# Kernel optimization log

Measured on AMD Instinct MI355X. Metric: run time of the kernel, lower is better.

The kernel has to match this reference:

```python
import jax, jax.numpy as jnp
import numpy as np
from jax import lax

B, E, D, N, R, K = 4, 768, 1536, 16, 48, 4
H, W = 16, 16
L = H * W
NDIR = 4


def _perms():
    idx = np.arange(L)
    idx_v = np.arange(L).reshape(H, W).T.reshape(-1)  # column-major (vertical) scan order
    perms = [idx, idx[::-1].copy(), idx_v, idx_v[::-1].copy()]
    invs = [np.argsort(p) for p in perms]
    return [jnp.asarray(p) for p in perms], [jnp.asarray(p) for p in invs]

PERMS, INVS = _perms()


def setup_inputs() -> dict:
    key = jax.random.key(0)
    ks = jax.random.split(key, 10)
    hidden_states = jax.random.normal(ks[0], (B, L, E), jnp.float32)
    in_proj_w = jax.random.normal(ks[1], (2 * D, E), jnp.float32) * 0.02
    out_proj_w = jax.random.normal(ks[2], (E, D), jnp.float32) * 0.02
    conv_w = jax.random.normal(ks[3], (NDIR, D, K), jnp.float32) * 0.1
    conv_b = jax.random.normal(ks[4], (NDIR, D), jnp.float32) * 0.1
    xproj_w = jax.random.normal(ks[5], (NDIR, R + 2 * N, D), jnp.float32) * 0.02
    dt_init_std = R ** -0.5
    dtproj_w = jax.random.uniform(ks[6], (NDIR, D, R), jnp.float32, -dt_init_std, dt_init_std)
    dt = jnp.exp(jax.random.uniform(ks[7], (NDIR, D), jnp.float32)
                 * (np.log(0.1) - np.log(0.001)) + np.log(0.001))
    dt = jnp.clip(dt, 1e-4, None)
    dtproj_b = dt + jnp.log(-jnp.expm1(-dt))  # inverse-softplus init as in the module
    A_log = jnp.broadcast_to(
        jnp.log(jnp.arange(1, N + 1, dtype=jnp.float32))[None, None, :], (NDIR, D, N)).copy()
    D_param = jnp.ones((NDIR, D), jnp.float32)
    return dict(hidden_states=hidden_states, in_proj_w=in_proj_w, out_proj_w=out_proj_w,
                conv_w=conv_w, conv_b=conv_b, xproj_w=xproj_w, dtproj_w=dtproj_w,
                dtproj_b=dtproj_b, A_log=A_log, D_param=D_param)


def _mamba_dir(xz, cw, cb, xw, dtw, dtb, a_log, dpar):
    # xz: (B, 2D, L) in this direction's scan order
    x, z = xz[:, :D], xz[:, D:]
    # causal depthwise conv1d + SiLU (mamba_inner_fn conv path)
    x = lax.conv_general_dilated(x, cw[:, None, :], (1,), [(K - 1, 0)],
                                 feature_group_count=D,
                                 dimension_numbers=('NCH', 'OIH', 'NCH'))
    x = jax.nn.silu(x + cb[None, :, None])
    # x_proj -> dt, B, C
    x_dbl = jnp.einsum('bdl,kd->bkl', x, xw)
    dt, Bm, Cm = x_dbl[:, :R], x_dbl[:, R:R + N], x_dbl[:, R + N:]
    delta = jax.nn.softplus(jnp.einsum('brl,dr->bdl', dt, dtw) + dtb[None, :, None])
    A = -jnp.exp(a_log)                                  # (D, N)
    dA = jnp.exp(jnp.einsum('bdl,dn->lbdn', delta, A))   # (L, B, D, N)
    dBu = jnp.einsum('bdl,bnl,bdl->lbdn', delta, Bm, x)  # delta * B * u

    def step(h, inp):
        da, dbu = inp
        h = da * h + dbu
        return h, h

    h0 = jnp.zeros((x.shape[0], D, N), x.dtype)
    _, hs = lax.scan(step, h0, (dA, dBu))                # (L, B, D, N)
    y = jnp.einsum('lbdn,bnl->bdl', hs, Cm) + dpar[None, :, None] * x
    return y * jax.nn.silu(z)                            # gate, (B, D, L)


def reference(hidden_states, in_proj_w, out_proj_w, conv_w, conv_b,
              xproj_w, dtproj_w, dtproj_b, A_log, D_param):
    xz = jnp.einsum('ble,fe->bfl', hidden_states, in_proj_w)  # (B, 2D, L)
    out = jnp.zeros((hidden_states.shape[0], D, L), hidden_states.dtype)
    for i in range(NDIR):  # fixed small set of structurally distinct scan directions
        xz_i = xz[:, :, PERMS[i]]
        y = _mamba_dir(xz_i, conv_w[i], conv_b[i], xproj_w[i], dtproj_w[i],
                       dtproj_b[i], A_log[i], D_param[i])
        out = out + y[:, :, INVS[i]]  # multi_reverse then sum-fusion
    return jnp.einsum('bdl,ed->ble', out, out_proj_w)
```

## Files before the change

### kernel.cpp

```cpp
#include <hip/hip_runtime.h>
#include <hip/hip_bf16.h>

#define BI   4
#define LI   256
#define EI   768
#define DI   1536
#define NI   16
#define RI   48
#define KI   4
#define NDIRS 4
#define F2D  3072
#define MROWS 1024
#define LOG2E 1.4426950408889634f

typedef float    floatx2 __attribute__((ext_vector_type(2)));
typedef float    floatx4 __attribute__((ext_vector_type(4)));
typedef _Float16 halfx2  __attribute__((ext_vector_type(2)));
typedef _Float16 halfx4  __attribute__((ext_vector_type(4)));
typedef _Float16 halfx8  __attribute__((ext_vector_type(8)));

typedef __attribute__((address_space(3))) unsigned lds_u32;
typedef __attribute__((address_space(1))) const unsigned glb_u32;

__device__ __forceinline__ void load16(const _Float16* g, _Float16* l) {
    __builtin_amdgcn_global_load_lds((glb_u32*)g, (lds_u32*)l, 16, 0, 0);
}

__device__ __forceinline__ int perm_idx(int dir, int j) {
    switch (dir) {
        case 0:  return j;
        case 1:  return 255 - j;
        case 2:  return ((j & 15) << 4) | (j >> 4);
        default: return 255 - (((j & 15) << 4) | (j >> 4));
    }
}

template<int CTRL>
__device__ __forceinline__ float dpp_add(float p) {
    int t = __builtin_amdgcn_update_dpp(0, __builtin_bit_cast(int, p),
                                        CTRL, 0xf, 0xf, true);
    return p + __builtin_bit_cast(float, t);
}
__device__ __forceinline__ float grp8_sum(float p) {
    p = dpp_add<0xB1>(p);
    p = dpp_add<0x4E>(p);
    p = dpp_add<0x141>(p);
    return p;
}

template<int BM, int BN, int WGN, int FM, int FN>
__device__ __forceinline__ void gemm_core(const _Float16* __restrict__ Ah,
                                          const _Float16* __restrict__ Al, int lda,
                                          const _Float16* __restrict__ Bh,
                                          const _Float16* __restrict__ Bl, int ldb,
                                          int nChunks, _Float16* smem,
                                          floatx4 (&acc)[FM][FN]) {
    const int tid = threadIdx.x, lane = tid & 63, wave = tid >> 6;
    const int wave_m = wave / WGN, wave_n = wave % WGN;
    _Float16* sAh = smem;
    _Float16* sAl = smem + BM * 32;
    _Float16* sBh = smem + BM * 64;
    _Float16* sBl = smem + BM * 64 + BN * 32;
    const int rr = lane & 15, koff = (lane >> 4) * 8;
    const int arow = wave_m * FM * 16, brow = wave_n * FN * 16;

    for (int c = 0; c < nChunks; ++c) {
        for (int idx = tid; idx < BM * 4; idx += 256) {
            int r = idx >> 2, s = (idx & 3) * 8;
            load16(Ah + (size_t)r * lda + c * 32 + s, sAh + idx * 8);
            load16(Al + (size_t)r * lda + c * 32 + s, sAl + idx * 8);
        }
        for (int idx = tid; idx < BN * 4; idx += 256) {
            int r = idx >> 2, s = (idx & 3) * 8;
            load16(Bh + (size_t)r * ldb + c * 32 + s, sBh + idx * 8);
            load16(Bl + (size_t)r * ldb + c * 32 + s, sBl + idx * 8);
        }
        asm volatile("s_waitcnt vmcnt(0)" ::: "memory");
        __syncthreads();

        halfx8 ahf[FM], alf[FM], bhf[FN], blf[FN];
        #pragma unroll
        for (int i = 0; i < FM; ++i) {
            ahf[i] = *(const halfx8*)(sAh + (arow + i * 16 + rr) * 32 + koff);
            alf[i] = *(const halfx8*)(sAl + (arow + i * 16 + rr) * 32 + koff);
        }
        #pragma unroll
        for (int j = 0; j < FN; ++j) {
            bhf[j] = *(const halfx8*)(sBh + (brow + j * 16 + rr) * 32 + koff);
            blf[j] = *(const halfx8*)(sBl + (brow + j * 16 + rr) * 32 + koff);
        }
        #pragma unroll
        for (int i = 0; i < FM; ++i)
            #pragma unroll
            for (int j = 0; j < FN; ++j) {
                acc[i][j] = __builtin_amdgcn_mfma_f32_16x16x32_f16(ahf[i], bhf[j], acc[i][j], 0, 0, 0);
                acc[i][j] = __builtin_amdgcn_mfma_f32_16x16x32_f16(ahf[i], blf[j], acc[i][j], 0, 0, 0);
                acc[i][j] = __builtin_amdgcn_mfma_f32_16x16x32_f16(alf[i], bhf[j], acc[i][j], 0, 0, 0);
            }
        __syncthreads();
    }
}

__global__ __launch_bounds__(256) void k_splitall(
        const float* __restrict__ hs,  const float* __restrict__ wip,
        const float* __restrict__ wop, const float* __restrict__ xw,
        const float* __restrict__ dtw,
        _Float16* __restrict__ hsh,  _Float16* __restrict__ hsl,
        _Float16* __restrict__ wiph, _Float16* __restrict__ wipl,
        _Float16* __restrict__ woph, _Float16* __restrict__ wopl,
        _Float16* __restrict__ xwh,  _Float16* __restrict__ xwl,
        _Float16* __restrict__ dtwh, _Float16* __restrict__ dtwl) {
    int i4 = (blockIdx.x * 256 + threadIdx.x) * 4;
    floatx4 v;
    _Float16 *dh, *dl; int off;
    if (i4 < 786432)        { off = i4;           v = *(const floatx4*)(hs + off);  dh = hsh;  dl = hsl;  }
    else if (i4 < 3145728)  { off = i4 - 786432;  v = *(const floatx4*)(wip + off); dh = wiph; dl = wipl; }
    else if (i4 < 4325376)  { off = i4 - 3145728; v = *(const floatx4*)(wop + off); dh = woph; dl = wopl; }
    else if (i4 < 4816896)  { off = i4 - 4325376; v = *(const floatx4*)(xw + off);  dh = xwh;  dl = xwl;  }
    else {
        int t0 = i4 - 4816896;
        int col = t0 & 63, dr = t0 >> 6;
        floatx4 z = {0.f, 0.f, 0.f, 0.f};
        v = (col < 48) ? *(const floatx4*)(dtw + (size_t)dr * 48 + col) : z;
        dh = dtwh; dl = dtwl; off = t0;
    }
    halfx4 hh, hl;
    #pragma unroll
    for (int e = 0; e < 4; ++e) {
        _Float16 h = (_Float16)v[e];
        hh[e] = h; hl[e] = (_Float16)(v[e] - (float)h);
    }
    *(halfx4*)(dh + off) = hh;
    *(halfx4*)(dl + off) = hl;
}

__global__ __launch_bounds__(256) void k_inproj_t(const _Float16* __restrict__ Ah,
                                                  const _Float16* __restrict__ Al,
                                                  const _Float16* __restrict__ Bh,
                                                  const _Float16* __restrict__ Bl,
                                                  float* __restrict__ C) {
    __shared__ _Float16 smem[128 * 64 + 128 * 64];
    int row0 = blockIdx.x * 128, col0 = blockIdx.y * 128, k0 = blockIdx.z * 384;
    float* Cp = C + (size_t)blockIdx.z * MROWS * F2D;
    floatx4 acc[4][4] = {};
    gemm_core<128, 128, 2, 4, 4>(Ah + (size_t)row0 * EI + k0, Al + (size_t)row0 * EI + k0, EI,
                                 Bh + (size_t)col0 * EI + k0, Bl + (size_t)col0 * EI + k0, EI,
                                 12, smem, acc);
    int lane = threadIdx.x & 63, wave = threadIdx.x >> 6;
    int cc = lane & 15, q = lane >> 4;
    int rbase = row0 + (wave >> 1) * 64, cbase = col0 + (wave & 1) * 64;
    #pragma unroll
    for (int i = 0; i < 4; ++i)
        #pragma unroll
        for (int j = 0; j < 4; ++j)
            #pragma unroll
            for (int r = 0; r < 4; ++r)
                Cp[(size_t)(rbase + i * 16 + q * 4 + r) * F2D + cbase + j * 16 + cc] = acc[i][j][r];
}

__global__ __launch_bounds__(256) void k_outproj_t(const _Float16* __restrict__ Ah,
                                                   const _Float16* __restrict__ Al,
                                                   const _Float16* __restrict__ Bh,
                                                   const _Float16* __restrict__ Bl,
                                                   float* __restrict__ C) {
    __shared__ _Float16 smem[192 * 64];
    int row0 = blockIdx.x * 64, col0 = blockIdx.y * 128, k0 = blockIdx.z * 384;
    float* Cp = C + (size_t)blockIdx.z * MROWS * EI;
    floatx4 acc[2][4] = {};
    gemm_core<64, 128, 2, 2, 4>(Ah + (size_t)row0 * DI + k0, Al + (size_t)row0 * DI + k0, DI,
                                Bh + (size_t)col0 * DI + k0, Bl + (size_t)col0 * DI + k0, DI,
                                12, smem, acc);
    int lane = threadIdx.x & 63, wave = threadIdx.x >> 6;
    int cc = lane & 15, q = lane >> 4;
    int rbase = row0 + (wave >> 1) * 32, cbase = col0 + (wave & 1) * 64;
    #pragma unroll
    for (int i = 0; i < 2; ++i)
        #pragma unroll
        for (int j = 0; j < 4; ++j)
            #pragma unroll
            for (int r = 0; r < 4; ++r)
                Cp[(size_t)(rbase + i * 16 + q * 4 + r) * EI + cbase + j * 16 + cc] = acc[i][j][r];
}

__global__ __launch_bounds__(256) void k_osum(const float* __restrict__ oacc,
                                              float* __restrict__ out) {
    int i4 = (blockIdx.x * 256 + threadIdx.x) * 4;
    const size_t S = (size_t)MROWS * EI;
    floatx4 s = *(const floatx4*)(oacc + i4) + *(const floatx4*)(oacc + S + i4) +
                *(const floatx4*)(oacc + 2 * S + i4) + *(const floatx4*)(oacc + 3 * S + i4);
    *(floatx4*)(out + i4) = s;
}

__global__ __launch_bounds__(256) void k_xdbl_t(const _Float16* __restrict__ xh,
                                                const _Float16* __restrict__ xl,
                                                const _Float16* __restrict__ xwh,
                                                const _Float16* __restrict__ xwl,
                                                float* __restrict__ C) {
    __shared__ _Float16 smem[208 * 64];
    int row0 = blockIdx.x * 128, dir = blockIdx.y, k0 = blockIdx.z * 192;
    float* Cp = C + (size_t)blockIdx.z * NDIRS * MROWS * 80;
    floatx4 acc[2][5] = {};
    const size_t abase = ((size_t)dir * MROWS + row0) * DI + k0;
    const size_t bbase = (size_t)dir * 80 * DI + k0;
    gemm_core<128, 80, 1, 2, 5>(xh + abase, xl + abase, DI,
                                xwh + bbase, xwl + bbase, DI, 6, smem, acc);
    int lane = threadIdx.x & 63, wave = threadIdx.x >> 6;
    int cc = lane & 15, q = lane >> 4;
    int rbase = row0 + wave * 32;
    #pragma unroll
    for (int i = 0; i < 2; ++i)
        #pragma unroll
        for (int j = 0; j < 5; ++j)
            #pragma unroll
            for (int r = 0; r < 4; ++r)
                Cp[((size_t)dir * MROWS + rbase + i * 16 + q * 4 + r) * 80 + j * 16 + cc] = acc[i][j][r];
}

__global__ __launch_bounds__(256) void k_xsplit(const float* __restrict__ acc,
                                                _Float16* __restrict__ dtqh,
                                                _Float16* __restrict__ dtql,
                                                float* __restrict__ BCm) {
    const size_t PS = (size_t)NDIRS * MROWS * 80;
    int idx = blockIdx.x * 256 + threadIdx.x;
    int dir = idx / (MROWS * 96);
    int rem = idx - dir * MROWS * 96;
    int row = rem / 96, col = rem - row * 96;
    size_t rbase = (size_t)dir * MROWS + row;
    auto sum8 = [&](int c) {
        size_t o = rbase * 80 + c;
        float s = 0.f;
        #pragma unroll
        for (int kp = 0; kp < 8; ++kp) s += acc[kp * PS + o];
        return s;
    };
    if (col < 64) {
        float v = (col < 48) ? sum8(col) : 0.f;
        _Float16 h = (_Float16)v;
        dtqh[rbase * 64 + col] = h;
        dtql[rbase * 64 + col] = (_Float16)(v - (float)h);
    } else if (col < 80) {
        int n = col - 64;
        BCm[rbase * 32 + n * 2] = sum8(48 + n);
    } else {
        int n = col - 80;
        BCm[rbase * 32 + n * 2 + 1] = sum8(64 + n);
    }
}

__global__ __launch_bounds__(256) void k_delta_t(const _Float16* __restrict__ dtqh,
                                                 const _Float16* __restrict__ dtql,
                                                 const _Float16* __restrict__ dtwh,
                                                 const _Float16* __restrict__ dtwl,
                                                 const float* __restrict__ dtb,
                                                 float* __restrict__ delta) {
    __shared__ _Float16 smem[192 * 64];
    int row0 = blockIdx.x * 64, col0 = blockIdx.y * 128, dir = blockIdx.z;
    floatx4 acc[2][4] = {};
    const size_t abase = ((size_t)dir * MROWS + row0) * 64;
    const size_t bbase = ((size_t)dir * DI + col0) * 64;
    gemm_core<64, 128, 2, 2, 4>(dtqh + abase, dtql + abase, 64,
                                dtwh + bbase, dtwl + bbase, 64, 2, smem, acc);
    int lane = threadIdx.x & 63, wave = threadIdx.x >> 6;
    int cc = lane & 15, q = lane >> 4;
    int rbase = row0 + (wave >> 1) * 32, cbase = col0 + (wave & 1) * 64;
    #pragma unroll
    for (int i = 0; i < 2; ++i)
        #pragma unroll
        for (int j = 0; j < 4; ++j) {
            int col = cbase + j * 16 + cc;
            float bias = dtb[(size_t)dir * DI + col];
            #pragma unroll
            for (int r = 0; r < 4; ++r) {
                float v = acc[i][j][r] + bias;
                float sp = (v > 20.f) ? v : log1pf(__expf(v));
                delta[((size_t)dir * MROWS + rbase + i * 16 + q * 4 + r) * DI + col] = sp;
            }
        }
}

__global__ __launch_bounds__(256) void k_conv(const float* __restrict__ xz,
                                              const float* __restrict__ cw,
                                              const float* __restrict__ cb,
                                              _Float16* __restrict__ xh,
                                              _Float16* __restrict__ xl) {
    const size_t S = (size_t)MROWS * F2D;
    int dir = blockIdx.z, b = blockIdx.y;
    int lchunk = blockIdx.x / 6, dsub = blockIdx.x % 6;
    int d = dsub * 256 + threadIdx.x;
    int base = lchunk * 16;

    const float* w = cw + ((size_t)dir * DI + d) * KI;
    float w0 = w[0], w1 = w[1], w2 = w[2], w3 = w[3];
    float bias = cb[(size_t)dir * DI + d];

    auto ld = [&](int m) -> float {
        if (m < 0) return 0.f;
        int src = perm_idx(dir, m);
        size_t o = ((size_t)b * 256 + src) * F2D + d;
        return xz[o] + xz[S + o];
    };
    float xm3 = ld(base - 3), xm2 = ld(base - 2), xm1 = ld(base - 1);

    #pragma unroll
    for (int j = 0; j < 16; ++j) {
        float cur = ld(base + j);
        float s = bias + w0 * xm3 + w1 * xm2 + w2 * xm1 + w3 * cur;
        xm3 = xm2; xm2 = xm1; xm1 = cur;
        float x = s / (1.f + __expf(-s));
        _Float16 h = (_Float16)x;
        size_t o = ((size_t)dir * MROWS + b * 256 + base + j) * DI + d;
        xh[o] = h;
        xl[o] = (_Float16)(x - (float)h);
    }
}

__global__ __launch_bounds__(256) void k_scan(const float* __restrict__ delta,
                                              const _Float16* __restrict__ xhg,
                                              const _Float16* __restrict__ xlg,
                                              const float* __restrict__ BCm,
                                              const float* __restrict__ A_log,
                                              const float* __restrict__ Dp,
                                              float* __restrict__ ydir) {
    const int dchunk = blockIdx.x, b = blockIdx.y, dir = blockIdx.z;
    const int tid = threadIdx.x;
    const int dslot = tid >> 3;
    const int np = tid & 7;
    const int d0 = dchunk * 32, d = d0 + dslot;

    __shared__ float sdx[2][32][64];
    __shared__ float sbc[2][32][32];
    __shared__ float sY[32][32];

    const float Av0 = -__expf(A_log[((size_t)dir * DI + d) * NI + 2 * np]) * LOG2E;
    const float Av1 = -__expf(A_log[((size_t)dir * DI + d) * NI + 2 * np + 1]) * LOG2E;
    const float Dpar = Dp[(size_t)dir * DI + d];
    float h0 = 0.f, h1 = 0.f;

    const size_t dirrow = (size_t)dir * MROWS;
    const int srow = tid >> 3, sc4 = (tid & 7) * 4;

    floatx4 rdel, rbc;
    halfx4 rxh, rxl;
    auto load_chunk = [&](int j0) {
        int row = b * 256 + j0 + srow;
        size_t o = (dirrow + row) * DI + d0 + sc4;
        rdel = *(const floatx4*)(delta + o);
        rxh  = *(const halfx4*)(xhg + o);
        rxl  = *(const halfx4*)(xlg + o);
        rbc  = *(const floatx4*)(BCm + (dirrow + row) * 32 + sc4);
    };

    load_chunk(0);

    for (int c = 0; c < 8; ++c) {
        const int buf = c & 1;
        #pragma unroll
        for (int e = 0; e < 4; ++e) {
            sdx[buf][srow][(sc4 + e) * 2]     = rdel[e];
            sdx[buf][srow][(sc4 + e) * 2 + 1] = (float)rxh[e] + (float)rxl[e];
        }
        *(floatx4*)&sbc[buf][srow][sc4] = rbc;
        __syncthreads();
        if (c < 7) load_chunk((c + 1) * 32);

        #pragma unroll
        for (int jj = 0; jj < 32; ++jj) {
            floatx2 dx = *(const floatx2*)&sdx[buf][jj][dslot * 2];
            floatx4 bc = *(const floatx4*)&sbc[buf][jj][np * 4];
            float dv = dx[0], xv = dx[1];
            float a0 = __builtin_amdgcn_exp2f(dv * Av0);
            float a1 = __builtin_amdgcn_exp2f(dv * Av1);
            float du = dv * xv;
            h0 = fmaf(a0, h0, du * bc[0]);
            h1 = fmaf(a1, h1, du * bc[2]);
            float p = fmaf(h1, bc[3], h0 * bc[1]);
            p = grp8_sum(p);
            if (np == 0) sY[jj][dslot] = fmaf(Dpar, xv, p);
        }
        __syncthreads();

        {
            int lout = perm_idx(dir, c * 32 + srow);
            floatx4 o = *(const floatx4*)&sY[srow][sc4];
            *(floatx4*)&ydir[(dirrow + (size_t)b * 256 + lout) * DI + d0 + sc4] = o;
        }
    }
}

__global__ __launch_bounds__(256) void k_sum(const float* __restrict__ ydir,
                                             const float* __restrict__ xz,
                                             _Float16* __restrict__ yh,
                                             _Float16* __restrict__ yl) {
    int i4 = (blockIdx.x * 256 + threadIdx.x) * 4;
    const size_t S = (size_t)MROWS * DI;
    const size_t SZ = (size_t)MROWS * F2D;
    int row = i4 / DI, dcol = i4 - row * DI;
    size_t zo = (size_t)row * F2D + DI + dcol;
    floatx4 zv = *(const floatx4*)(xz + zo) + *(const floatx4*)(xz + SZ + zo);
    floatx4 s = *(const floatx4*)(ydir + i4) + *(const floatx4*)(ydir + S + i4) +
                *(const floatx4*)(ydir + 2 * S + i4) + *(const floatx4*)(ydir + 3 * S + i4);
    halfx4 hh, hl;
    #pragma unroll
    for (int e = 0; e < 4; ++e) {
        float g = zv[e] / (1.f + __expf(-zv[e]));
        float v = s[e] * g;
        _Float16 h = (_Float16)v;
        hh[e] = h; hl[e] = (_Float16)(v - (float)h);
    }
    *(halfx4*)(yh + i4) = hh;
    *(halfx4*)(yl + i4) = hl;
}

extern "C" void kernel_launch(void* const* d_in, const int* in_sizes, int n_in,
                              void* d_out, int out_size, void* d_ws, size_t ws_size,
                              hipStream_t stream) {
    const float* hs   = (const float*)d_in[0];
    const float* wip  = (const float*)d_in[1];
    const float* wop  = (const float*)d_in[2];
    const float* cw   = (const float*)d_in[3];
    const float* cb   = (const float*)d_in[4];
    const float* xw   = (const float*)d_in[5];
    const float* dtw  = (const float*)d_in[6];
    const float* dtb  = (const float*)d_in[7];
    const float* alog = (const float*)d_in[8];
    const float* dpar = (const float*)d_in[9];
    float* out = (float*)d_out;

    char* p = (char*)d_ws;
    auto alloc_f32 = [&](size_t n) { float* r = (float*)p; p += n * 4; return r; };
    auto alloc_f16 = [&](size_t n) { _Float16* r = (_Float16*)p; p += n * 2; return r; };

    _Float16* hsh  = alloc_f16(786432);
    _Float16* hsl  = alloc_f16(786432);
    _Float16* wiph = alloc_f16(2359296);
    _Float16* wipl = alloc_f16(2359296);
    _Float16* woph = alloc_f16(1179648);
    _Float16* wopl = alloc_f16(1179648);
    _Float16* xwh  = alloc_f16(491520);
    _Float16* xwl  = alloc_f16(491520);
    _Float16* dtwh = alloc_f16((size_t)NDIRS * DI * 64);
    _Float16* dtwl = alloc_f16((size_t)NDIRS * DI * 64);
    float*    xz   = alloc_f32((size_t)2 * MROWS * F2D);
    _Float16* xh   = alloc_f16((size_t)NDIRS * MROWS * DI);
    _Float16* xl   = alloc_f16((size_t)NDIRS * MROWS * DI);
    _Float16* dtqh = alloc_f16((size_t)NDIRS * MROWS * 64);
    _Float16* dtql = alloc_f16((size_t)NDIRS * MROWS * 64);
    float*    BCm  = alloc_f32((size_t)NDIRS * MROWS * 32);
    float*    delta= alloc_f32((size_t)NDIRS * MROWS * DI);
    float*    ydir = alloc_f32((size_t)NDIRS * MROWS * DI);
    _Float16* yh   = alloc_f16((size_t)MROWS * DI);
    _Float16* yl   = alloc_f16((size_t)MROWS * DI);

    float* xdba = ydir;
    float* oacc = delta;

    k_splitall<<<dim3(5088), 256, 0, stream>>>(hs, wip, wop, xw, dtw,
                                               hsh, hsl, wiph, wipl, woph, wopl,
                                               xwh, xwl, dtwh, dtwl);
    k_inproj_t<<<dim3(8, 24, 2), 256, 0, stream>>>(hsh, hsl, wiph, wipl, xz);
    k_conv    <<<dim3(96, BI, NDIRS), 256, 0, stream>>>(xz, cw, cb, xh, xl);
    k_xdbl_t  <<<dim3(8, NDIRS, 8), 256, 0, stream>>>(xh, xl, xwh, xwl, xdba);
    k_xsplit  <<<dim3(1536), 256, 0, stream>>>(xdba, dtqh, dtql, BCm);
    k_delta_t <<<dim3(16, 12, NDIRS), 256, 0, stream>>>(dtqh, dtql, dtwh, dtwl, dtb, delta);
    k_scan    <<<dim3(DI / 32, BI, NDIRS), 256, 0, stream>>>(delta, xh, xl, BCm,
                                                             alog, dpar, ydir);
    k_sum     <<<dim3(1536), 256, 0, stream>>>(ydir, xz, yh, yl);
    k_outproj_t<<<dim3(16, 6, 4), 256, 0, stream>>>(yh, yl, woph, wopl, oacc);
    k_osum    <<<dim3(768), 256, 0, stream>>>(oacc, out);
}
```

Measured before the change: 227.6 us.

## Share conv input across directions via LDS and transpose scan delta/x tile

The conv kernel now loads each (batch, 16-channel) slice of the summed xz once into shared memory and computes all four scan directions from it, instead of re-reading the permuted global data separately per direction. Its stores become narrow 16-channel segments, and it launches fewer blocks with 512 threads each. The scan kernel stores its delta/x tile transposed with padding so each thread reads two timesteps with a single vector LDS load. The cost is a transposed LDS write pattern that may cause bank conflicts.

Measured after the change: 231.8 us. About the same (+1.8%).

```diff
diff --git a/kernel.cpp b/kernel.cpp
--- a/kernel.cpp
+++ b/kernel.cpp
@@ -278,39 +278,46 @@
         }
 }
 
-__global__ __launch_bounds__(256) void k_conv(const float* __restrict__ xz,
-                                              const float* __restrict__ cw,
-                                              const float* __restrict__ cb,
-                                              _Float16* __restrict__ xh,
-                                              _Float16* __restrict__ xl) {
+__global__ __launch_bounds__(512) void k_conv4(const float* __restrict__ xz,
+                                               const float* __restrict__ cw,
+                                               const float* __restrict__ cb,
+                                               _Float16* __restrict__ xh,
+                                               _Float16* __restrict__ xl) {
     const size_t S = (size_t)MROWS * F2D;
-    int dir = blockIdx.z, b = blockIdx.y;
-    int lchunk = blockIdx.x / 6, dsub = blockIdx.x % 6;
-    int d = dsub * 256 + threadIdx.x;
-    int base = lchunk * 16;
-
-    const float* w = cw + ((size_t)dir * DI + d) * KI;
-    float w0 = w[0], w1 = w[1], w2 = w[2], w3 = w[3];
-    float bias = cb[(size_t)dir * DI + d];
-
-    auto ld = [&](int m) -> float {
-        if (m < 0) return 0.f;
-        int src = perm_idx(dir, m);
-        size_t o = ((size_t)b * 256 + src) * F2D + d;
-        return xz[o] + xz[S + o];
-    };
-    float xm3 = ld(base - 3), xm2 = ld(base - 2), xm1 = ld(base - 1);
-
-    #pragma unroll
-    for (int j = 0; j < 16; ++j) {
-        float cur = ld(base + j);
-        float s = bias + w0 * xm3 + w1 * xm2 + w2 * xm1 + w3 * cur;
-        xm3 = xm2; xm2 = xm1; xm1 = cur;
-        float x = s / (1.f + __expf(-s));
-        _Float16 h = (_Float16)x;
-        size_t o = ((size_t)dir * MROWS + b * 256 + base + j) * DI + d;
-        xh[o] = h;
-        xl[o] = (_Float16)(x - (float)h);
+    const int b = blockIdx.y, d0 = blockIdx.x * 16;
+    const int tid = threadIdx.x;
+    __shared__ float sx[256][18];
+
+    for (int i = tid; i < 1024; i += 512) {
+        int row = i >> 2, c4 = (i & 3) * 4;
+        size_t o = ((size_t)b * 256 + row) * F2D + d0 + c4;
+        floatx4 v = *(const floatx4*)(xz + o) + *(const floatx4*)(xz + S + o);
+        floatx2 v0 = {v[0], v[1]}, v1 = {v[2], v[3]};
+        *(floatx2*)&sx[row][c4]     = v0;
+        *(floatx2*)&sx[row][c4 + 2] = v1;
+    }
+    __syncthreads();
+
+    const int dsub = tid & 15, lg = tid >> 4;
+    const int d = d0 + dsub, j0 = lg * 8;
+    #pragma unroll
+    for (int dir = 0; dir < NDIRS; ++dir) {
+        floatx4 w = *(const floatx4*)(cw + ((size_t)dir * DI + d) * KI);
+        float bias = cb[(size_t)dir * DI + d];
+        float xm3 = (j0 >= 3) ? sx[perm_idx(dir, j0 - 3)][dsub] : 0.f;
+        float xm2 = (j0 >= 2) ? sx[perm_idx(dir, j0 - 2)][dsub] : 0.f;
+        float xm1 = (j0 >= 1) ? sx[perm_idx(dir, j0 - 1)][dsub] : 0.f;
+        #pragma unroll
+        for (int j = 0; j < 8; ++j) {
+            float cur = sx[perm_idx(dir, j0 + j)][dsub];
+            float s = bias + w[0] * xm3 + w[1] * xm2 + w[2] * xm1 + w[3] * cur;
+            xm3 = xm2; xm2 = xm1; xm1 = cur;
+            float x = s / (1.f + __expf(-s));
+            _Float16 h = (_Float16)x;
+            size_t o = ((size_t)dir * MROWS + b * 256 + j0 + j) * DI + d;
+            xh[o] = h;
+            xl[o] = (_Float16)(x - (float)h);
+        }
     }
 }
 
@@ -327,7 +334,7 @@
     const int np = tid & 7;
     const int d0 = dchunk * 32, d = d0 + dslot;
 
-    __shared__ float sdx[2][32][64];
+    __shared__ float sdx[2][32][68];
     __shared__ float sbc[2][32][32];
     __shared__ float sY[32][32];
 
@@ -356,26 +363,31 @@
         const int buf = c & 1;
         #pragma unroll
         for (int e = 0; e < 4; ++e) {
-            sdx[buf][srow][(sc4 + e) * 2]     = rdel[e];
-            sdx[buf][srow][(sc4 + e) * 2 + 1] = (float)rxh[e] + (float)rxl[e];
+            floatx2 t;
+            t[0] = rdel[e];
+            t[1] = (float)rxh[e] + (float)rxl[e];
+            *(floatx2*)&sdx[buf][sc4 + e][srow * 2] = t;
         }
         *(floatx4*)&sbc[buf][srow][sc4] = rbc;
         __syncthreads();
         if (c < 7) load_chunk((c + 1) * 32);
 
         #pragma unroll
-        for (int jj = 0; jj < 32; ++jj) {
-            floatx2 dx = *(const floatx2*)&sdx[buf][jj][dslot * 2];
-            floatx4 bc = *(const floatx4*)&sbc[buf][jj][np * 4];
-            float dv = dx[0], xv = dx[1];
-            float a0 = __builtin_amdgcn_exp2f(dv * Av0);
-            float a1 = __builtin_amdgcn_exp2f(dv * Av1);
-            float du = dv * xv;
-            h0 = fmaf(a0, h0, du * bc[0]);
-            h1 = fmaf(a1, h1, du * bc[2]);
-            float p = fmaf(h1, bc[3], h0 * bc[1]);
-            p = grp8_sum(p);
-            if (np == 0) sY[jj][dslot] = fmaf(Dpar, xv, p);
+        for (int jj = 0; jj < 32; jj += 2) {
+            floatx4 dxx = *(const floatx4*)&sdx[buf][dslot][jj * 2];
+            #pragma unroll
+            for (int t = 0; t < 2; ++t) {
+                floatx4 bc = *(const floatx4*)&sbc[buf][jj + t][np * 4];
+                float dv = dxx[t * 2], xv = dxx[t * 2 + 1];
+                float a0 = __builtin_amdgcn_exp2f(dv * Av0);
+                float a1 = __builtin_amdgcn_exp2f(dv * Av1);
+                float du = dv * xv;
+                h0 = fmaf(a0, h0, du * bc[0]);
+                h1 = fmaf(a1, h1, du * bc[2]);
+                float p = fmaf(h1, bc[3], h0 * bc[1]);
+                p = grp8_sum(p);
+                if (np == 0) sY[jj + t][dslot] = fmaf(Dpar, xv, p);
+            }
         }
         __syncthreads();
 
@@ -458,7 +470,7 @@
                                                hsh, hsl, wiph, wipl, woph, wopl,
                                                xwh, xwl, dtwh, dtwl);
     k_inproj_t<<<dim3(8, 24, 2), 256, 0, stream>>>(hsh, hsl, wiph, wipl, xz);
-    k_conv    <<<dim3(96, BI, NDIRS), 256, 0, stream>>>(xz, cw, cb, xh, xl);
+    k_conv4   <<<dim3(96, BI), 512, 0, stream>>>(xz, cw, cb, xh, xl);
     k_xdbl_t  <<<dim3(8, NDIRS, 8), 256, 0, stream>>>(xh, xl, xwh, xwl, xdba);
     k_xsplit  <<<dim3(1536), 256, 0, stream>>>(xdba, dtqh, dtql, BCm);
     k_delta_t <<<dim3(16, 12, NDIRS), 256, 0, stream>>>(dtqh, dtql, dtwh, dtwl, dtb, delta);
```
